# Optimization experiments

Hardware: AMD Instinct MI355X
Metric: run time of the kernel (lower is better)

The kernel has to match this reference:

```python
import jax, jax.numpy as jnp
import numpy as np


def setup_inputs() -> dict:
    key = jax.random.key(0)
    k1, k2 = jax.random.split(key)
    B, H, W, C = 32, 32, 32, 256
    N_EMBED = 1024
    z = jax.random.normal(k1, (B, H, W, C), dtype=jnp.float32)
    emb_weights = jax.random.normal(k2, (N_EMBED, C), dtype=jnp.float32)
    return {"z": z, "emb_weights": emb_weights}


def reference(z, emb_weights):
    # z: (B,H,W,C) -> flatten to (N, C)
    B = z.shape[0]
    C = z.shape[-1]
    z_flat = z.reshape(-1, C)  # (N, C)
    # Squared euclidean distance via ||z||^2 + ||e||^2 - 2 z.e^T
    distance = (
        jnp.sum(z_flat ** 2, axis=1, keepdims=True)          # (N, 1)
        + jnp.sum(emb_weights ** 2, axis=1)                   # (n_embed,)
        - 2.0 * jnp.dot(z_flat, emb_weights.T)                # (N, n_embed)
    )
    min_encoding_indices = jnp.argmin(distance, axis=1)       # (N,)
    z_q = emb_weights[min_encoding_indices].reshape(z.shape)  # (B,H,W,C)
    min_encoding_indices = min_encoding_indices.reshape(B, -1)
    return z_q, min_encoding_indices
```

## Files before the change

### kernel.cpp

```cpp
#include <hip/hip_runtime.h>

#define C_DIM 256
#define NCODE 1024
#define MARGIN1 0.35f
#define MARGIN2 0.02f

typedef __bf16 bf16x8 __attribute__((ext_vector_type(8)));
typedef float f32x4 __attribute__((ext_vector_type(4)));

#define WS_ENORM  0
#define WS_META   4096
#define WS_RLIST  8192
#define WS_RLIST2 139264
#define WS_BP     270336
#define WS_PB     1318912
#define WS_PBI    1843200

#define BP_LO_OFF 262144

#define GLOAD_LDS16(g, s)                                                            \
  __builtin_amdgcn_global_load_lds(                                                  \
      (const __attribute__((address_space(1))) unsigned int*)(g),                    \
      (__attribute__((address_space(3))) unsigned int*)(s), 16, 0, 0)

__device__ __forceinline__ unsigned short bf16rne(float x) {
    unsigned u = __float_as_uint(x);
    return (unsigned short)((u + 0x7FFFu + ((u >> 16) & 1u)) >> 16);
}
__device__ __forceinline__ void bf16split(float x, unsigned short& h, unsigned short& l) {
    unsigned u  = __float_as_uint(x);
    unsigned rh = (u + 0x7FFFu + ((u >> 16) & 1u)) & 0xFFFF0000u;
    float    lf = x - __uint_as_float(rh);
    h = (unsigned short)(rh >> 16);
    l = bf16rne(lf);
}

__global__ __launch_bounds__(256) void prep_kernel(const float* __restrict__ emb,
                                                   unsigned short* __restrict__ bp,
                                                   float* __restrict__ enorm,
                                                   unsigned* __restrict__ meta) {
    int tid = blockIdx.x * 256 + threadIdx.x;
    if (tid < 2) meta[tid] = 0u;
    int j   = tid >> 5;
    int u   = tid & 31;
    int kc  = u >> 2, lg = u & 3;
    const float* src = emb + (size_t)j * C_DIM + kc * 32 + lg * 8;
    float4 v0 = *reinterpret_cast<const float4*>(src);
    float4 v1 = *reinterpret_cast<const float4*>(src + 4);
    float vs[8] = {v0.x, v0.y, v0.z, v0.w, v1.x, v1.y, v1.z, v1.w};
    unsigned short h[8], l[8];
    float s = 0.f;
    #pragma unroll
    for (int k = 0; k < 8; ++k) {
        bf16split(vs[k], h[k], l[k]);
        s = fmaf(vs[k], vs[k], s);
    }
    #pragma unroll
    for (int off = 1; off < 32; off <<= 1) s += __shfl_xor(s, off, 64);
    if (u == 0) enorm[j] = s;

    int chunk = j >> 5, nf = (j >> 4) & 1, lr = j & 15;
    int lane  = lg * 16 + lr;
    size_t base = (size_t)chunk * 8192 + (size_t)(nf * 8 + kc) * 512 + lane * 8;
    uint4 hp, lp;
    hp.x = (unsigned)h[0] | ((unsigned)h[1] << 16);
    hp.y = (unsigned)h[2] | ((unsigned)h[3] << 16);
    hp.z = (unsigned)h[4] | ((unsigned)h[5] << 16);
    hp.w = (unsigned)h[6] | ((unsigned)h[7] << 16);
    lp.x = (unsigned)l[0] | ((unsigned)l[1] << 16);
    lp.y = (unsigned)l[2] | ((unsigned)l[3] << 16);
    lp.z = (unsigned)l[4] | ((unsigned)l[5] << 16);
    lp.w = (unsigned)l[6] | ((unsigned)l[7] << 16);
    *reinterpret_cast<uint4*>(bp + base)             = hp;
    *reinterpret_cast<uint4*>(bp + BP_LO_OFF + base) = lp;
}

__global__ __launch_bounds__(256, 3) void vq_stage1_kernel(
    const float* __restrict__ z, const unsigned short* __restrict__ bp,
    const float* __restrict__ enorm, float2* __restrict__ pb,
    unsigned* __restrict__ pbi) {
    __shared__ unsigned short Bds[3][8192];
    __shared__ float en_s[512];

    const int t = threadIdx.x;
    const int w = t >> 6, lane = t & 63;
    const int lr = lane & 15, lg = lane >> 4;
    const int nh = blockIdx.x & 1;
    const long r0 = (long)(blockIdx.x >> 1) * 128 + w * 32;
    const unsigned short* bsrc = bp + (size_t)(nh * 16) * 8192 + lane * 8;

    en_s[t]       = enorm[nh * 512 + t];
    en_s[t + 256] = enorm[nh * 512 + 256 + t];

    bf16x8 ah[2][8];
    #pragma unroll
    for (int m = 0; m < 2; ++m) {
        const float* zr = z + (r0 + m * 16 + lr) * C_DIM + lg * 8;
        #pragma unroll
        for (int kc = 0; kc < 8; ++kc) {
            float4 v0 = *reinterpret_cast<const float4*>(zr + kc * 32);
            float4 v1 = *reinterpret_cast<const float4*>(zr + kc * 32 + 4);
            float vs[8] = {v0.x, v0.y, v0.z, v0.w, v1.x, v1.y, v1.z, v1.w};
            unsigned hp[4];
            #pragma unroll
            for (int p = 0; p < 4; ++p)
                hp[p] = (unsigned)bf16rne(vs[2 * p]) |
                        ((unsigned)bf16rne(vs[2 * p + 1]) << 16);
            ah[m][kc] = __builtin_bit_cast(bf16x8, *reinterpret_cast<uint4*>(hp));
        }
    }
    __syncthreads();

#define STG1(c, sl) {                                                   \
    unsigned short* db = &Bds[sl][0];                                   \
    const unsigned short* gs = bsrc + (size_t)(c) * 8192;               \
    _Pragma("unroll") for (int rd = 0; rd < 4; ++rd) {                  \
        int s_ = rd * 4 + w;                                            \
        GLOAD_LDS16(gs + s_ * 512, db + s_ * 512); } }

    STG1(0, 0); STG1(1, 1);

    float b1[2][4], b2[2][4]; unsigned i1[2][4];
    #pragma unroll
    for (int m = 0; m < 2; ++m)
        #pragma unroll
        for (int r = 0; r < 4; ++r) { b1[m][r] = 3.4e38f; b2[m][r] = 3.4e38f; i1[m][r] = 0; }

    int rs = 0, ws = 2;
    #pragma unroll 1
    for (int c = 0; c < 16; ++c) {
        if (c <= 14) { asm volatile("s_waitcnt vmcnt(4)" ::: "memory"); }
        else         { asm volatile("s_waitcnt vmcnt(0)" ::: "memory"); }
        __builtin_amdgcn_s_barrier();
        if (c < 14) STG1(c + 2, ws);

        f32x4 a00 = {0.f,0.f,0.f,0.f}, a01 = {0.f,0.f,0.f,0.f};
        f32x4 a10 = {0.f,0.f,0.f,0.f}, a11 = {0.f,0.f,0.f,0.f};
        const unsigned short* bb = &Bds[rs][lane * 8];
        __builtin_amdgcn_s_setprio(1);
        #pragma unroll
        for (int kc = 0; kc < 8; ++kc) {
            bf16x8 bh0 = *reinterpret_cast<const bf16x8*>(bb + kc * 512);
            bf16x8 bh1 = *reinterpret_cast<const bf16x8*>(bb + (8 + kc) * 512);
            a00 = __builtin_amdgcn_mfma_f32_16x16x32_bf16(ah[0][kc], bh0, a00, 0, 0, 0);
            a10 = __builtin_amdgcn_mfma_f32_16x16x32_bf16(ah[1][kc], bh0, a10, 0, 0, 0);
            a01 = __builtin_amdgcn_mfma_f32_16x16x32_bf16(ah[0][kc], bh1, a01, 0, 0, 0);
            a11 = __builtin_amdgcn_mfma_f32_16x16x32_bf16(ah[1][kc], bh1, a11, 0, 0, 0);
        }
        __builtin_amdgcn_s_setprio(0);

        #pragma unroll
        for (int nf = 0; nf < 2; ++nf) {
            const int cl = c * 32 + nf * 16 + lr;
            const float en = en_s[cl];
            const unsigned code = (unsigned)(nh * 512 + cl);
            #pragma unroll
            for (int r = 0; r < 4; ++r) {
                float d0 = fmaf(-2.f, (nf ? a01[r] : a00[r]), en);
                if (d0 < b1[0][r]) { b2[0][r] = b1[0][r]; b1[0][r] = d0; i1[0][r] = code; }
                else if (d0 < b2[0][r]) { b2[0][r] = d0; }
                float d1 = fmaf(-2.f, (nf ? a11[r] : a10[r]), en);
                if (d1 < b1[1][r]) { b2[1][r] = b1[1][r]; b1[1][r] = d1; i1[1][r] = code; }
                else if (d1 < b2[1][r]) { b2[1][r] = d1; }
            }
        }
        rs = rs + 1; if (rs == 3) rs = 0;
        ws = ws + 1; if (ws == 3) ws = 0;
    }
#undef STG1

    #pragma unroll
    for (int m = 0; m < 2; ++m)
        #pragma unroll
        for (int r = 0; r < 4; ++r) {
            float v1 = b1[m][r], v2 = b2[m][r]; unsigned j1 = i1[m][r];
            #pragma unroll
            for (int off = 8; off; off >>= 1) {
                float    ov1 = __shfl_xor(v1, off, 64);
                float    ov2 = __shfl_xor(v2, off, 64);
                unsigned oj1 = (unsigned)__shfl_xor((int)j1, off, 64);
                if (ov1 < v1 || (ov1 == v1 && oj1 < j1)) {
                    v2 = fminf(v1, ov2); v1 = ov1; j1 = oj1;
                } else {
                    v2 = fminf(v2, ov1);
                }
            }
            if (lr == 0) {
                long row = r0 + m * 16 + lg * 4 + r;
                pb [row * 2 + nh] = make_float2(v1, v2);
                pbi[row * 2 + nh] = j1;
            }
        }
}

__global__ __launch_bounds__(256) void finalize_gather_kernel(
    const float* __restrict__ emb, const float2* __restrict__ pb,
    const unsigned* __restrict__ pbi, float* __restrict__ zq,
    float* __restrict__ idx_out, unsigned* __restrict__ meta,
    unsigned* __restrict__ rlist, int n4) {
    const int lane = threadIdx.x & 63;
    for (long r4 = blockIdx.x; r4 < n4; r4 += gridDim.x) {
        const long row = r4 * 4 + (threadIdx.x >> 6);
        float2   p0 = pb [row * 2 + 0], p1 = pb [row * 2 + 1];
        unsigned j0 = pbi[row * 2 + 0], j1 = pbi[row * 2 + 1];
        float B1, B2; unsigned I1;
        if (p1.x < p0.x) { B1 = p1.x; I1 = j1; B2 = fminf(p0.x, p1.y); }
        else             { B1 = p0.x; I1 = j0; B2 = fminf(p0.y, p1.x); }
        if (lane == 0) {
            idx_out[row] = (float)I1;
            if (B2 - B1 <= MARGIN1) rlist[atomicAdd(meta, 1u)] = (unsigned)row;
        }
        float4 v = reinterpret_cast<const float4*>(emb)[(size_t)I1 * 64 + lane];
        reinterpret_cast<float4*>(zq)[row * 64 + lane] = v;
    }
}

__global__ __launch_bounds__(256) void vq_stage2_kernel(
    const float* __restrict__ z, const unsigned short* __restrict__ bp,
    const float* __restrict__ enorm, const float* __restrict__ emb,
    const unsigned* __restrict__ meta, const unsigned* __restrict__ rlist,
    float* __restrict__ zq, float* __restrict__ idx_out,
    unsigned* __restrict__ meta2, unsigned* __restrict__ rlist2) {
    __shared__ float en_s[NCODE];
    __shared__ float m1s[16][4], m2s[16][4];
    __shared__ unsigned mis[16][4];
    __shared__ unsigned codes_s[16];
    const int t = threadIdx.x, q = t >> 6, lane = t & 63;
    const int lr = lane & 15, lg = lane >> 4;
    en_s[t] = enorm[t]; en_s[t + 256] = enorm[t + 256];
    en_s[t + 512] = enorm[t + 512]; en_s[t + 768] = enorm[t + 768];
    __syncthreads();
    const unsigned cnt = meta[0];
    const unsigned ngroups = (cnt + 15) >> 4;

    for (unsigned g = blockIdx.x; g < ngroups; g += gridDim.x) {
        const unsigned base = g * 16;
        unsigned slot = base + (unsigned)lr;
        unsigned row = rlist[slot < cnt ? slot : 0];

        bf16x8 ah[8], al[8];
        const float* zr = z + (size_t)row * C_DIM + lg * 8;
        #pragma unroll
        for (int kc = 0; kc < 8; ++kc) {
            float4 v0 = *reinterpret_cast<const float4*>(zr + kc * 32);
            float4 v1 = *reinterpret_cast<const float4*>(zr + kc * 32 + 4);
            float vs[8] = {v0.x, v0.y, v0.z, v0.w, v1.x, v1.y, v1.z, v1.w};
            unsigned short hv[8], lv[8];
            #pragma unroll
            for (int jj = 0; jj < 8; ++jj) bf16split(vs[jj], hv[jj], lv[jj]);
            unsigned hp[4] = {
                (unsigned)hv[0] | ((unsigned)hv[1] << 16), (unsigned)hv[2] | ((unsigned)hv[3] << 16),
                (unsigned)hv[4] | ((unsigned)hv[5] << 16), (unsigned)hv[6] | ((unsigned)hv[7] << 16)};
            unsigned lp[4] = {
                (unsigned)lv[0] | ((unsigned)lv[1] << 16), (unsigned)lv[2] | ((unsigned)lv[3] << 16),
                (unsigned)lv[4] | ((unsigned)lv[5] << 16), (unsigned)lv[6] | ((unsigned)lv[7] << 16)};
            ah[kc] = __builtin_bit_cast(bf16x8, *reinterpret_cast<uint4*>(hp));
            al[kc] = __builtin_bit_cast(bf16x8, *reinterpret_cast<uint4*>(lp));
        }

        float b1[4], b2[4]; unsigned i1[4];
        #pragma unroll
        for (int r = 0; r < 4; ++r) { b1[r] = 3.4e38f; b2[r] = 3.4e38f; i1[r] = 0; }

        #pragma unroll 1
        for (int cc = 0; cc < 8; ++cc) {
            const int c = q * 8 + cc;
            f32x4 hh0 = {0.f,0.f,0.f,0.f}, hh1 = {0.f,0.f,0.f,0.f};
            f32x4 hl0 = {0.f,0.f,0.f,0.f}, hl1 = {0.f,0.f,0.f,0.f};
            f32x4 lh0 = {0.f,0.f,0.f,0.f}, lh1 = {0.f,0.f,0.f,0.f};
            const unsigned short* cb = bp + (size_t)c * 8192 + lane * 8;
            #pragma unroll
            for (int kc = 0; kc < 8; ++kc) {
                bf16x8 bh0 = *reinterpret_cast<const bf16x8*>(cb + kc * 512);
                bf16x8 bh1 = *reinterpret_cast<const bf16x8*>(cb + (8 + kc) * 512);
                bf16x8 bl0 = *reinterpret_cast<const bf16x8*>(cb + BP_LO_OFF + kc * 512);
                bf16x8 bl1 = *reinterpret_cast<const bf16x8*>(cb + BP_LO_OFF + (8 + kc) * 512);
                hh0 = __builtin_amdgcn_mfma_f32_16x16x32_bf16(ah[kc], bh0, hh0, 0, 0, 0);
                hh1 = __builtin_amdgcn_mfma_f32_16x16x32_bf16(ah[kc], bh1, hh1, 0, 0, 0);
                lh0 = __builtin_amdgcn_mfma_f32_16x16x32_bf16(al[kc], bh0, lh0, 0, 0, 0);
                lh1 = __builtin_amdgcn_mfma_f32_16x16x32_bf16(al[kc], bh1, lh1, 0, 0, 0);
                hl0 = __builtin_amdgcn_mfma_f32_16x16x32_bf16(ah[kc], bl0, hl0, 0, 0, 0);
                hl1 = __builtin_amdgcn_mfma_f32_16x16x32_bf16(ah[kc], bl1, hl1, 0, 0, 0);
            }
            #pragma unroll
            for (int nf = 0; nf < 2; ++nf) {
                const unsigned code = (unsigned)(c * 32 + nf * 16 + lr);
                const float en = en_s[code];
                #pragma unroll
                for (int r = 0; r < 4; ++r) {
                    float s3 = nf ? (hh1[r] + hl1[r] + lh1[r]) : (hh0[r] + hl0[r] + lh0[r]);
                    float d = fmaf(-2.f, s3, en);
                    if (d < b1[r]) { b2[r] = b1[r]; b1[r] = d; i1[r] = code; }
                    else if (d < b2[r]) { b2[r] = d; }
                }
            }
        }

        #pragma unroll
        for (int r = 0; r < 4; ++r) {
            float v1 = b1[r], v2 = b2[r]; unsigned j1 = i1[r];
            #pragma unroll
            for (int off = 8; off; off >>= 1) {
                float    ov1 = __shfl_xor(v1, off, 64);
                float    ov2 = __shfl_xor(v2, off, 64);
                unsigned oj1 = (unsigned)__shfl_xor((int)j1, off, 64);
                if (ov1 < v1 || (ov1 == v1 && oj1 < j1)) {
                    v2 = fminf(v1, ov2); v1 = ov1; j1 = oj1;
                } else {
                    v2 = fminf(v2, ov1);
                }
            }
            if (lr == 0) {
                int rg = lg * 4 + r;
                m1s[rg][q] = v1; m2s[rg][q] = v2; mis[rg][q] = j1;
            }
        }
        __syncthreads();
        if (t < 16) {
            float B1 = 3.4e38f, B2 = 3.4e38f; unsigned I1 = 0;
            #pragma unroll
            for (int s = 0; s < 4; ++s) {
                float v1 = m1s[t][s], v2 = m2s[t][s]; unsigned j = mis[t][s];
                if (v1 < B1) { B2 = fminf(B1, v2); B1 = v1; I1 = j; }
                else         { B2 = fminf(B2, v1); }
            }
            unsigned sl = base + (unsigned)t;
            codes_s[t] = I1;
            if (sl < cnt) {
                unsigned rrow = rlist[sl];
                idx_out[rrow] = (float)I1;
                if (B2 - B1 <= MARGIN2) rlist2[atomicAdd(meta2, 1u)] = rrow;
            }
        }
        __syncthreads();
        {
            int rr = t >> 4, seg = t & 15;
            unsigned sl = base + (unsigned)rr;
            if (sl < cnt) {
                unsigned rrow = rlist[sl];
                unsigned code = codes_s[rr];
                const float4* ep = reinterpret_cast<const float4*>(emb) + (size_t)code * 64 + seg * 4;
                float4*       op = reinterpret_cast<float4*>(zq) + (size_t)rrow * 64 + seg * 4;
                op[0] = ep[0]; op[1] = ep[1]; op[2] = ep[2]; op[3] = ep[3];
            }
        }
        __syncthreads();
    }
}

__global__ __launch_bounds__(256) void rescue_kernel(
    const float* __restrict__ z, const float* __restrict__ emb,
    const float* __restrict__ enorm, const unsigned* __restrict__ meta2,
    const unsigned* __restrict__ rlist2, float* __restrict__ zq,
    float* __restrict__ idx_out) {
    __shared__ float zrow[C_DIM];
    __shared__ float rd[256];
    __shared__ unsigned rix[256];
    const unsigned cnt = meta2[0];
    for (unsigned li = blockIdx.x; li < cnt; li += gridDim.x) {
        unsigned row = rlist2[li];
        __syncthreads();
        if (threadIdx.x < 64) {
            float4 v = reinterpret_cast<const float4*>(z)[(size_t)row * 64 + threadIdx.x];
            reinterpret_cast<float4*>(zrow)[threadIdx.x] = v;
        }
        __syncthreads();
        const int c = threadIdx.x;
        float a0 = 0.f, a1 = 0.f, a2 = 0.f, a3 = 0.f;
        const float4* zp = reinterpret_cast<const float4*>(zrow);
        const float4* e0 = reinterpret_cast<const float4*>(emb + (size_t)(c)       * C_DIM);
        const float4* e1 = reinterpret_cast<const float4*>(emb + (size_t)(c + 256) * C_DIM);
        const float4* e2 = reinterpret_cast<const float4*>(emb + (size_t)(c + 512) * C_DIM);
        const float4* e3 = reinterpret_cast<const float4*>(emb + (size_t)(c + 768) * C_DIM);
        #pragma unroll 8
        for (int k = 0; k < 64; ++k) {
            float4 z4 = zp[k];
            float4 f0 = e0[k], f1 = e1[k], f2 = e2[k], f3 = e3[k];
            a0 = fmaf(z4.x, f0.x, a0); a0 = fmaf(z4.y, f0.y, a0);
            a0 = fmaf(z4.z, f0.z, a0); a0 = fmaf(z4.w, f0.w, a0);
            a1 = fmaf(z4.x, f1.x, a1); a1 = fmaf(z4.y, f1.y, a1);
            a1 = fmaf(z4.z, f1.z, a1); a1 = fmaf(z4.w, f1.w, a1);
            a2 = fmaf(z4.x, f2.x, a2); a2 = fmaf(z4.y, f2.y, a2);
            a2 = fmaf(z4.z, f2.z, a2); a2 = fmaf(z4.w, f2.w, a2);
            a3 = fmaf(z4.x, f3.x, a3); a3 = fmaf(z4.y, f3.y, a3);
            a3 = fmaf(z4.z, f3.z, a3); a3 = fmaf(z4.w, f3.w, a3);
        }
        float d0 = fmaf(-2.f, a0, enorm[c]);
        float d1 = fmaf(-2.f, a1, enorm[c + 256]);
        float d2 = fmaf(-2.f, a2, enorm[c + 512]);
        float d3 = fmaf(-2.f, a3, enorm[c + 768]);
        float bd = d0; unsigned bi = (unsigned)c;
        if (d1 < bd) { bd = d1; bi = (unsigned)(c + 256); }
        if (d2 < bd) { bd = d2; bi = (unsigned)(c + 512); }
        if (d3 < bd) { bd = d3; bi = (unsigned)(c + 768); }
        rd[threadIdx.x] = bd; rix[threadIdx.x] = bi;
        __syncthreads();
        for (int s = 128; s; s >>= 1) {
            if (threadIdx.x < (unsigned)s) {
                float od = rd[threadIdx.x + s]; unsigned oi = rix[threadIdx.x + s];
                if (od < rd[threadIdx.x] ||
                    (od == rd[threadIdx.x] && oi < rix[threadIdx.x])) {
                    rd[threadIdx.x] = od; rix[threadIdx.x] = oi;
                }
            }
            __syncthreads();
        }
        unsigned code = rix[0];
        if (threadIdx.x < 64) {
            float4 v = reinterpret_cast<const float4*>(emb)[(size_t)code * 64 + threadIdx.x];
            reinterpret_cast<float4*>(zq)[(size_t)row * 64 + threadIdx.x] = v;
        }
        if (threadIdx.x == 0) idx_out[row] = (float)code;
    }
}

extern "C" void kernel_launch(void* const* d_in, const int* in_sizes, int n_in,
                              void* d_out, int out_size, void* d_ws, size_t ws_size,
                              hipStream_t stream) {
    const float* z   = (const float*)d_in[0];
    const float* emb = (const float*)d_in[1];
    const int n = in_sizes[0] / C_DIM;

    float* zq      = (float*)d_out;
    float* idx_out = zq + (size_t)n * C_DIM;

    char* ws = (char*)d_ws;
    float*          enorm  = (float*)(ws + WS_ENORM);
    unsigned*       meta   = (unsigned*)(ws + WS_META);
    unsigned*       rlist  = (unsigned*)(ws + WS_RLIST);
    unsigned*       rlist2 = (unsigned*)(ws + WS_RLIST2);
    unsigned short* bp     = (unsigned short*)(ws + WS_BP);
    float2*         pb     = (float2*)(ws + WS_PB);
    unsigned*       pbi    = (unsigned*)(ws + WS_PBI);

    prep_kernel<<<128, 256, 0, stream>>>(emb, bp, enorm, meta);
    vq_stage1_kernel<<<(n / 128) * 2, 256, 0, stream>>>(z, bp, enorm, pb, pbi);
    finalize_gather_kernel<<<2048, 256, 0, stream>>>(emb, pb, pbi, zq, idx_out,
                                                     meta, rlist, n / 4);
    vq_stage2_kernel<<<256, 256, 0, stream>>>(z, bp, enorm, emb, meta, rlist,
                                              zq, idx_out, meta + 1, rlist2);
    rescue_kernel<<<256, 256, 0, stream>>>(z, emb, enorm, meta + 1, rlist2,
                                           zq, idx_out);
}
```

Before: 134.0 us.

## Split codebook into quarters per stage-1 block with double-buffered LDS

Stage 1 now splits the 1024-entry codebook into four 256-code quarters per row tile instead of two halves. This doubles the grid and cuts the LDS pipeline from triple to double buffering, so occupancy can rise from 3 to 4 blocks per CU. Finalize merges four partial top-2 results per row, and the workspace offset is enlarged to fit them. The cost is that each row's z tile is loaded and converted to bf16 twice as often, the double buffer has less latency hiding (it waits on vmcnt(0) every iteration), and finalize does more partial-result traffic.

```diff
diff --git a/kernel.cpp b/kernel.cpp
--- a/kernel.cpp
+++ b/kernel.cpp
@@ -14,7 +14,7 @@
 #define WS_RLIST2 139264
 #define WS_BP     270336
 #define WS_PB     1318912
-#define WS_PBI    1843200
+#define WS_PBI    2367488
 
 #define BP_LO_OFF 262144
 
@@ -75,22 +75,21 @@
     *reinterpret_cast<uint4*>(bp + BP_LO_OFF + base) = lp;
 }
 
-__global__ __launch_bounds__(256, 3) void vq_stage1_kernel(
+__global__ __launch_bounds__(256, 4) void vq_stage1_kernel(
     const float* __restrict__ z, const unsigned short* __restrict__ bp,
     const float* __restrict__ enorm, float2* __restrict__ pb,
     unsigned* __restrict__ pbi) {
-    __shared__ unsigned short Bds[3][8192];
-    __shared__ float en_s[512];
+    __shared__ unsigned short Bds[2][8192];
+    __shared__ float en_s[256];
 
     const int t = threadIdx.x;
     const int w = t >> 6, lane = t & 63;
     const int lr = lane & 15, lg = lane >> 4;
-    const int nh = blockIdx.x & 1;
-    const long r0 = (long)(blockIdx.x >> 1) * 128 + w * 32;
-    const unsigned short* bsrc = bp + (size_t)(nh * 16) * 8192 + lane * 8;
-
-    en_s[t]       = enorm[nh * 512 + t];
-    en_s[t + 256] = enorm[nh * 512 + 256 + t];
+    const int nq = blockIdx.x & 3;
+    const long r0 = (long)(blockIdx.x >> 2) * 128 + w * 32;
+    const unsigned short* bsrc = bp + (size_t)(nq * 8) * 8192 + lane * 8;
+
+    en_s[t] = enorm[nq * 256 + t];
 
     bf16x8 ah[2][8];
     #pragma unroll
@@ -118,7 +117,7 @@
         int s_ = rd * 4 + w;                                            \
         GLOAD_LDS16(gs + s_ * 512, db + s_ * 512); } }
 
-    STG1(0, 0); STG1(1, 1);
+    STG1(0, 0);
 
     float b1[2][4], b2[2][4]; unsigned i1[2][4];
     #pragma unroll
@@ -126,17 +125,15 @@
         #pragma unroll
         for (int r = 0; r < 4; ++r) { b1[m][r] = 3.4e38f; b2[m][r] = 3.4e38f; i1[m][r] = 0; }
 
-    int rs = 0, ws = 2;
     #pragma unroll 1
-    for (int c = 0; c < 16; ++c) {
-        if (c <= 14) { asm volatile("s_waitcnt vmcnt(4)" ::: "memory"); }
-        else         { asm volatile("s_waitcnt vmcnt(0)" ::: "memory"); }
+    for (int c = 0; c < 8; ++c) {
+        asm volatile("s_waitcnt vmcnt(0)" ::: "memory");
         __builtin_amdgcn_s_barrier();
-        if (c < 14) STG1(c + 2, ws);
+        if (c < 7) STG1(c + 1, (c + 1) & 1);
 
         f32x4 a00 = {0.f,0.f,0.f,0.f}, a01 = {0.f,0.f,0.f,0.f};
         f32x4 a10 = {0.f,0.f,0.f,0.f}, a11 = {0.f,0.f,0.f,0.f};
-        const unsigned short* bb = &Bds[rs][lane * 8];
+        const unsigned short* bb = &Bds[c & 1][lane * 8];
         __builtin_amdgcn_s_setprio(1);
         #pragma unroll
         for (int kc = 0; kc < 8; ++kc) {
@@ -153,7 +150,7 @@
         for (int nf = 0; nf < 2; ++nf) {
             const int cl = c * 32 + nf * 16 + lr;
             const float en = en_s[cl];
-            const unsigned code = (unsigned)(nh * 512 + cl);
+            const unsigned code = (unsigned)(nq * 256 + cl);
             #pragma unroll
             for (int r = 0; r < 4; ++r) {
                 float d0 = fmaf(-2.f, (nf ? a01[r] : a00[r]), en);
@@ -164,8 +161,6 @@
                 else if (d1 < b2[1][r]) { b2[1][r] = d1; }
             }
         }
-        rs = rs + 1; if (rs == 3) rs = 0;
-        ws = ws + 1; if (ws == 3) ws = 0;
     }
 #undef STG1
 
@@ -187,8 +182,8 @@
             }
             if (lr == 0) {
                 long row = r0 + m * 16 + lg * 4 + r;
-                pb [row * 2 + nh] = make_float2(v1, v2);
-                pbi[row * 2 + nh] = j1;
+                pb [row * 4 + nq] = make_float2(v1, v2);
+                pbi[row * 4 + nq] = j1;
             }
         }
 }
@@ -201,11 +196,14 @@
     const int lane = threadIdx.x & 63;
     for (long r4 = blockIdx.x; r4 < n4; r4 += gridDim.x) {
         const long row = r4 * 4 + (threadIdx.x >> 6);
-        float2   p0 = pb [row * 2 + 0], p1 = pb [row * 2 + 1];
-        unsigned j0 = pbi[row * 2 + 0], j1 = pbi[row * 2 + 1];
-        float B1, B2; unsigned I1;
-        if (p1.x < p0.x) { B1 = p1.x; I1 = j1; B2 = fminf(p0.x, p1.y); }
-        else             { B1 = p0.x; I1 = j0; B2 = fminf(p0.y, p1.x); }
+        float B1 = 3.4e38f, B2 = 3.4e38f; unsigned I1 = 0;
+        #pragma unroll
+        for (int s = 0; s < 4; ++s) {
+            float2   p = pb [row * 4 + s];
+            unsigned j = pbi[row * 4 + s];
+            if (p.x < B1) { B2 = fminf(B1, p.y); B1 = p.x; I1 = j; }
+            else          { B2 = fminf(B2, p.x); }
+        }
         if (lane == 0) {
             idx_out[row] = (float)I1;
             if (B2 - B1 <= MARGIN1) rlist[atomicAdd(meta, 1u)] = (unsigned)row;
@@ -434,7 +432,7 @@
     unsigned*       pbi    = (unsigned*)(ws + WS_PBI);
 
     prep_kernel<<<128, 256, 0, stream>>>(emb, bp, enorm, meta);
-    vq_stage1_kernel<<<(n / 128) * 2, 256, 0, stream>>>(z, bp, enorm, pb, pbi);
+    vq_stage1_kernel<<<(n / 128) * 4, 256, 0, stream>>>(z, bp, enorm, pb, pbi);
     finalize_gather_kernel<<<2048, 256, 0, stream>>>(emb, pb, pbi, zq, idx_out,
                                                      meta, rlist, n / 4);
     vq_stage2_kernel<<<256, 256, 0, stream>>>(z, bp, enorm, emb, meta, rlist,
```

Measured after the change: 135.5 us. Within noise of the previous version (+1.1%).

## Fuse fp32 rescue pass into stage2 kernel using per-block shared rescue list

Applied to the files above, without the earlier changes.

Merges the separate rescue kernel into the stage-2 refinement kernel. Each block keeps the rows it could not resolve in a shared-memory list and recomputes them in exact fp32 right away, reading codebook norms from LDS. This drops one kernel launch and the global atomic list. The stage-2 gather is also rewritten so each wavefront copies one row with coalesced float4 accesses. The trade-off is load imbalance: blocks that get many ambiguous rows serialize their rescue work, and the extra shared memory may lower occupancy.

```diff
diff --git a/kernel.cpp b/kernel.cpp
--- a/kernel.cpp
+++ b/kernel.cpp
@@ -11,11 +11,9 @@
 #define WS_ENORM  0
 #define WS_META   4096
 #define WS_RLIST  8192
-#define WS_RLIST2 139264
 #define WS_BP     270336
 #define WS_PB     1318912
 #define WS_PBI    1843200
-
 #define BP_LO_OFF 262144
 
 #define GLOAD_LDS16(g, s)                                                            \
@@ -40,7 +38,7 @@
                                                    float* __restrict__ enorm,
                                                    unsigned* __restrict__ meta) {
     int tid = blockIdx.x * 256 + threadIdx.x;
-    if (tid < 2) meta[tid] = 0u;
+    if (tid == 0) meta[0] = 0u;
     int j   = tid >> 5;
     int u   = tid & 31;
     int kc  = u >> 2, lg = u & 3;
@@ -215,16 +213,20 @@
     }
 }
 
-__global__ __launch_bounds__(256) void vq_stage2_kernel(
+__global__ __launch_bounds__(256) void vq_stage2_rescue_kernel(
     const float* __restrict__ z, const unsigned short* __restrict__ bp,
     const float* __restrict__ enorm, const float* __restrict__ emb,
     const unsigned* __restrict__ meta, const unsigned* __restrict__ rlist,
-    float* __restrict__ zq, float* __restrict__ idx_out,
-    unsigned* __restrict__ meta2, unsigned* __restrict__ rlist2) {
+    float* __restrict__ zq, float* __restrict__ idx_out) {
     __shared__ float en_s[NCODE];
     __shared__ float m1s[16][4], m2s[16][4];
     __shared__ unsigned mis[16][4];
     __shared__ unsigned codes_s[16];
+    __shared__ unsigned resc_r[16];
+    __shared__ unsigned resc_n;
+    __shared__ float zrow[C_DIM];
+    __shared__ float rd[256];
+    __shared__ unsigned rix[256];
     const int t = threadIdx.x, q = t >> 6, lane = t & 63;
     const int lr = lane & 15, lg = lane >> 4;
     en_s[t] = enorm[t]; en_s[t + 256] = enorm[t + 256];
@@ -237,6 +239,7 @@
         const unsigned base = g * 16;
         unsigned slot = base + (unsigned)lr;
         unsigned row = rlist[slot < cnt ? slot : 0];
+        if (t == 0) resc_n = 0u;
 
         bf16x8 ah[8], al[8];
         const float* zr = z + (size_t)row * C_DIM + lg * 8;
@@ -329,88 +332,81 @@
             if (sl < cnt) {
                 unsigned rrow = rlist[sl];
                 idx_out[rrow] = (float)I1;
-                if (B2 - B1 <= MARGIN2) rlist2[atomicAdd(meta2, 1u)] = rrow;
+                if (B2 - B1 <= MARGIN2) resc_r[atomicAdd(&resc_n, 1u)] = rrow;
             }
         }
         __syncthreads();
         {
-            int rr = t >> 4, seg = t & 15;
-            unsigned sl = base + (unsigned)rr;
-            if (sl < cnt) {
-                unsigned rrow = rlist[sl];
-                unsigned code = codes_s[rr];
-                const float4* ep = reinterpret_cast<const float4*>(emb) + (size_t)code * 64 + seg * 4;
-                float4*       op = reinterpret_cast<float4*>(zq) + (size_t)rrow * 64 + seg * 4;
-                op[0] = ep[0]; op[1] = ep[1]; op[2] = ep[2]; op[3] = ep[3];
+            #pragma unroll
+            for (int it = 0; it < 4; ++it) {
+                int rr = it * 4 + q;
+                unsigned sl = base + (unsigned)rr;
+                if (sl < cnt) {
+                    unsigned rrow = rlist[sl];
+                    unsigned code = codes_s[rr];
+                    float4 v = reinterpret_cast<const float4*>(emb)[(size_t)code * 64 + lane];
+                    reinterpret_cast<float4*>(zq)[(size_t)rrow * 64 + lane] = v;
+                }
             }
         }
         __syncthreads();
-    }
-}
-
-__global__ __launch_bounds__(256) void rescue_kernel(
-    const float* __restrict__ z, const float* __restrict__ emb,
-    const float* __restrict__ enorm, const unsigned* __restrict__ meta2,
-    const unsigned* __restrict__ rlist2, float* __restrict__ zq,
-    float* __restrict__ idx_out) {
-    __shared__ float zrow[C_DIM];
-    __shared__ float rd[256];
-    __shared__ unsigned rix[256];
-    const unsigned cnt = meta2[0];
-    for (unsigned li = blockIdx.x; li < cnt; li += gridDim.x) {
-        unsigned row = rlist2[li];
+
+        const unsigned nresc = resc_n;
+        for (unsigned ri = 0; ri < nresc; ++ri) {
+            unsigned rrow = resc_r[ri];
+            if (t < 64) {
+                float4 v = reinterpret_cast<const float4*>(z)[(size_t)rrow * 64 + t];
+                reinterpret_cast<float4*>(zrow)[t] = v;
+            }
+            __syncthreads();
+            const int c = t;
+            float a0 = 0.f, a1 = 0.f, a2 = 0.f, a3 = 0.f;
+            const float4* zp = reinterpret_cast<const float4*>(zrow);
+            const float4* e0 = reinterpret_cast<const float4*>(emb + (size_t)(c)       * C_DIM);
+            const float4* e1 = reinterpret_cast<const float4*>(emb + (size_t)(c + 256) * C_DIM);
+            const float4* e2 = reinterpret_cast<const float4*>(emb + (size_t)(c + 512) * C_DIM);
+            const float4* e3 = reinterpret_cast<const float4*>(emb + (size_t)(c + 768) * C_DIM);
+            #pragma unroll 8
+            for (int k = 0; k < 64; ++k) {
+                float4 z4 = zp[k];
+                float4 f0 = e0[k], f1 = e1[k], f2 = e2[k], f3 = e3[k];
+                a0 = fmaf(z4.x, f0.x, a0); a0 = fmaf(z4.y, f0.y, a0);
+                a0 = fmaf(z4.z, f0.z, a0); a0 = fmaf(z4.w, f0.w, a0);
+                a1 = fmaf(z4.x, f1.x, a1); a1 = fmaf(z4.y, f1.y, a1);
+                a1 = fmaf(z4.z, f1.z, a1); a1 = fmaf(z4.w, f1.w, a1);
+                a2 = fmaf(z4.x, f2.x, a2); a2 = fmaf(z4.y, f2.y, a2);
+                a2 = fmaf(z4.z, f2.z, a2); a2 = fmaf(z4.w, f2.w, a2);
+                a3 = fmaf(z4.x, f3.x, a3); a3 = fmaf(z4.y, f3.y, a3);
+                a3 = fmaf(z4.z, f3.z, a3); a3 = fmaf(z4.w, f3.w, a3);
+            }
+            float d0 = fmaf(-2.f, a0, en_s[c]);
+            float d1 = fmaf(-2.f, a1, en_s[c + 256]);
+            float d2 = fmaf(-2.f, a2, en_s[c + 512]);
+            float d3 = fmaf(-2.f, a3, en_s[c + 768]);
+            float bd = d0; unsigned bi = (unsigned)c;
+            if (d1 < bd) { bd = d1; bi = (unsigned)(c + 256); }
+            if (d2 < bd) { bd = d2; bi = (unsigned)(c + 512); }
+            if (d3 < bd) { bd = d3; bi = (unsigned)(c + 768); }
+            rd[t] = bd; rix[t] = bi;
+            __syncthreads();
+            for (int s = 128; s; s >>= 1) {
+                if (t < s) {
+                    float od = rd[t + s]; unsigned oi = rix[t + s];
+                    if (od < rd[t] || (od == rd[t] && oi < rix[t])) {
+                        rd[t] = od; rix[t] = oi;
+                    }
+                }
+                __syncthreads();
+            }
+            unsigned code = rix[0];
+            if (t < 64) {
+                float4 v = reinterpret_cast<const float4*>(emb)[(size_t)code * 64 + t];
+                reinterpret_cast<float4*>(zq)[(size_t)rrow * 64 + t] = v;
+            }
+            if (t == 0) idx_out[rrow] = (float)code;
+            __syncthreads();
+        }
         __syncthreads();
-        if (threadIdx.x < 64) {
-            float4 v = reinterpret_cast<const float4*>(z)[(size_t)row * 64 + threadIdx.x];
-            reinterpret_cast<float4*>(zrow)[threadIdx.x] = v;
-        }
-        __syncthreads();
-        const int c = threadIdx.x;
-        float a0 = 0.f, a1 = 0.f, a2 = 0.f, a3 = 0.f;
-        const float4* zp = reinterpret_cast<const float4*>(zrow);
-        const float4* e0 = reinterpret_cast<const float4*>(emb + (size_t)(c)       * C_DIM);
-        const float4* e1 = reinterpret_cast<const float4*>(emb + (size_t)(c + 256) * C_DIM);
-        const float4* e2 = reinterpret_cast<const float4*>(emb + (size_t)(c + 512) * C_DIM);
-        const float4* e3 = reinterpret_cast<const float4*>(emb + (size_t)(c + 768) * C_DIM);
-        #pragma unroll 8
-        for (int k = 0; k < 64; ++k) {
-            float4 z4 = zp[k];
-            float4 f0 = e0[k], f1 = e1[k], f2 = e2[k], f3 = e3[k];
-            a0 = fmaf(z4.x, f0.x, a0); a0 = fmaf(z4.y, f0.y, a0);
-            a0 = fmaf(z4.z, f0.z, a0); a0 = fmaf(z4.w, f0.w, a0);
-            a1 = fmaf(z4.x, f1.x, a1); a1 = fmaf(z4.y, f1.y, a1);
-            a1 = fmaf(z4.z, f1.z, a1); a1 = fmaf(z4.w, f1.w, a1);
-            a2 = fmaf(z4.x, f2.x, a2); a2 = fmaf(z4.y, f2.y, a2);
-            a2 = fmaf(z4.z, f2.z, a2); a2 = fmaf(z4.w, f2.w, a2);
-            a3 = fmaf(z4.x, f3.x, a3); a3 = fmaf(z4.y, f3.y, a3);
-            a3 = fmaf(z4.z, f3.z, a3); a3 = fmaf(z4.w, f3.w, a3);
-        }
-        float d0 = fmaf(-2.f, a0, enorm[c]);
-        float d1 = fmaf(-2.f, a1, enorm[c + 256]);
-        float d2 = fmaf(-2.f, a2, enorm[c + 512]);
-        float d3 = fmaf(-2.f, a3, enorm[c + 768]);
-        float bd = d0; unsigned bi = (unsigned)c;
-        if (d1 < bd) { bd = d1; bi = (unsigned)(c + 256); }
-        if (d2 < bd) { bd = d2; bi = (unsigned)(c + 512); }
-        if (d3 < bd) { bd = d3; bi = (unsigned)(c + 768); }
-        rd[threadIdx.x] = bd; rix[threadIdx.x] = bi;
-        __syncthreads();
-        for (int s = 128; s; s >>= 1) {
-            if (threadIdx.x < (unsigned)s) {
-                float od = rd[threadIdx.x + s]; unsigned oi = rix[threadIdx.x + s];
-                if (od < rd[threadIdx.x] ||
-                    (od == rd[threadIdx.x] && oi < rix[threadIdx.x])) {
-                    rd[threadIdx.x] = od; rix[threadIdx.x] = oi;
-                }
-            }
-            __syncthreads();
-        }
-        unsigned code = rix[0];
-        if (threadIdx.x < 64) {
-            float4 v = reinterpret_cast<const float4*>(emb)[(size_t)code * 64 + threadIdx.x];
-            reinterpret_cast<float4*>(zq)[(size_t)row * 64 + threadIdx.x] = v;
-        }
-        if (threadIdx.x == 0) idx_out[row] = (float)code;
     }
 }
 
@@ -425,20 +421,17 @@
     float* idx_out = zq + (size_t)n * C_DIM;
 
     char* ws = (char*)d_ws;
-    float*          enorm  = (float*)(ws + WS_ENORM);
-    unsigned*       meta   = (unsigned*)(ws + WS_META);
-    unsigned*       rlist  = (unsigned*)(ws + WS_RLIST);
-    unsigned*       rlist2 = (unsigned*)(ws + WS_RLIST2);
-    unsigned short* bp     = (unsigned short*)(ws + WS_BP);
-    float2*         pb     = (float2*)(ws + WS_PB);
-    unsigned*       pbi    = (unsigned*)(ws + WS_PBI);
+    float*          enorm = (float*)(ws + WS_ENORM);
+    unsigned*       meta  = (unsigned*)(ws + WS_META);
+    unsigned*       rlist = (unsigned*)(ws + WS_RLIST);
+    unsigned short* bp    = (unsigned short*)(ws + WS_BP);
+    float2*         pb    = (float2*)(ws + WS_PB);
+    unsigned*       pbi   = (unsigned*)(ws + WS_PBI);
 
     prep_kernel<<<128, 256, 0, stream>>>(emb, bp, enorm, meta);
     vq_stage1_kernel<<<(n / 128) * 2, 256, 0, stream>>>(z, bp, enorm, pb, pbi);
     finalize_gather_kernel<<<2048, 256, 0, stream>>>(emb, pb, pbi, zq, idx_out,
                                                      meta, rlist, n / 4);
-    vq_stage2_kernel<<<256, 256, 0, stream>>>(z, bp, enorm, emb, meta, rlist,
-                                              zq, idx_out, meta + 1, rlist2);
-    rescue_kernel<<<256, 256, 0, stream>>>(z, emb, enorm, meta + 1, rlist2,
-                                           zq, idx_out);
-}
+    vq_stage2_rescue_kernel<<<256, 256, 0, stream>>>(z, bp, enorm, emb, meta,
+                                                     rlist, zq, idx_out);
+}
```

Result: slower. 211.4 us (+57.8%).
